# Performance work log

Hardware: AMD Instinct MI355X
Metric: run time of the kernel (lower is better)

Reference implementation:

```python
import jax, jax.numpy as jnp
import numpy as np

B, SM, SI, D, H, FF = 4, 1024, 4096, 256, 8, 1024
EPS = 1e-6

def _ln(x, g, b):
    m = jnp.mean(x, axis=-1, keepdims=True)
    v = jnp.mean(jnp.square(x - m), axis=-1, keepdims=True)
    return (x - m) * jax.lax.rsqrt(v + EPS) * g + b

def setup_inputs() -> dict:
    key = jax.random.key(0)
    ks = jax.random.split(key, 12)
    s = 0.02
    return {
        "state_seq": jax.random.normal(ks[0], (B, SM, D), jnp.float32),
        "input_seq": jax.random.normal(ks[1], (B, SI, D), jnp.float32),
        "Wk": jax.random.normal(ks[2], (D, D), jnp.float32) * s,
        "bk": jnp.zeros((D,), jnp.float32),
        "Wv": jax.random.normal(ks[3], (D, D), jnp.float32) * s,
        "bv": jnp.zeros((D,), jnp.float32),
        "Wq": jax.random.normal(ks[4], (H, D, D), jnp.float32) * s,
        "bq": jnp.zeros((H, D), jnp.float32),
        "Wo": jax.random.normal(ks[5], (H * D, D), jnp.float32) * s,
        "bo": jnp.zeros((D,), jnp.float32),
        "ln1_g": jnp.ones((D,), jnp.float32),
        "ln1_b": jnp.zeros((D,), jnp.float32),
        "W_in": jax.random.normal(ks[6], (D, FF), jnp.float32) * s,
        "b_in": jnp.zeros((FF,), jnp.float32),
        "Wg_nl": jax.random.normal(ks[7], (FF, FF), jnp.float32) * s,
        "bg_nl": jnp.zeros((FF,), jnp.float32),
        "Wg_l": jax.random.normal(ks[8], (FF, FF), jnp.float32) * s,
        "bg_l": jnp.zeros((FF,), jnp.float32),
        "Wg_o": jax.random.normal(ks[9], (FF, D), jnp.float32) * s,
        "bg_o": jnp.zeros((D,), jnp.float32),
        "ln2_g": jnp.ones((D,), jnp.float32),
        "ln2_b": jnp.zeros((D,), jnp.float32),
    }

def reference(state_seq, input_seq, Wk, bk, Wv, bv, Wq, bq, Wo, bo,
              ln1_g, ln1_b, W_in, b_in, Wg_nl, bg_nl, Wg_l, bg_l, Wg_o, bg_o,
              ln2_g, ln2_b):
    # shared key/value projections (multi-query: one K/V, many Q)
    ik = input_seq @ Wk + bk            # [B,SI,D]
    mk = state_seq @ Wk + bk            # [B,SM,D]
    iv = input_seq @ Wv + bv            # [B,SI,D]
    mv = state_seq @ Wv + bv            # [B,SM,D]
    # per-head queries from memory cells, stacked over H
    q = jnp.einsum('bmd,hde->hbme', state_seq, Wq) + bq[:, None, None, :]  # [H,B,SM,D]
    input_score = jnp.einsum('hbme,bse->hbms', q, ik)                      # [H,B,SM,SI]
    self_score = jnp.sum(q * mk[None], axis=-1, keepdims=True)             # [H,B,SM,1]
    score = jnp.concatenate([self_score, input_score], axis=-1)
    score = score / jnp.sqrt(jnp.asarray(D, score.dtype))
    attn = jax.nn.softmax(score, axis=-1)                                  # [H,B,SM,1+SI]
    val = jnp.einsum('hbms,bse->hbme', attn[..., 1:], iv) + attn[..., 0:1] * mv[None]
    concat = jnp.transpose(val, (1, 2, 0, 3)).reshape(val.shape[1], val.shape[2], -1)  # [B,SM,H*D]
    attn_out = concat @ Wo + bo
    x = _ln(attn_out + state_seq, ln1_g, ln1_b)
    h = jax.nn.relu(x @ W_in + b_in)                                       # [B,SM,FF]
    g = jax.nn.relu(h @ Wg_nl + bg_nl) * (h @ Wg_l + bg_l)
    ff = g @ Wg_o + bg_o
    return _ln(ff + x, ln2_g, ln2_b)
```

## Files before the change

kernel.cpp:

```cpp
#include <hip/hip_runtime.h>
#include <hip/hip_bf16.h>

typedef __bf16 bfx8 __attribute__((ext_vector_type(8)));
typedef __bf16 bfx4 __attribute__((ext_vector_type(4)));
typedef float  f32x4 __attribute__((ext_vector_type(4)));
typedef float  f32x16 __attribute__((ext_vector_type(16)));

#define MFMA16(a,b,c) __builtin_amdgcn_mfma_f32_16x16x32_bf16((a),(b),(c),0,0,0)
#define MFMA32(a,b,c) __builtin_amdgcn_mfma_f32_32x32x16_bf16((a),(b),(c),0,0,0)


#define PSCALE 0.09016844f
#define PCLAMP 43.2808512f

__device__ __forceinline__ unsigned cvtpk_bf16(float lo, float hi) {
  unsigned d;
  asm("v_cvt_pk_bf16_f32 %0, %1, %2" : "=v"(d) : "v"(lo), "v"(hi));
  return d;
}

__device__ __forceinline__ bfx8 packswap(const float* p) {
  unsigned a = cvtpk_bf16(p[0], p[1]);
  unsigned b = cvtpk_bf16(p[2], p[3]);
  unsigned c = cvtpk_bf16(p[4], p[5]);
  unsigned d = cvtpk_bf16(p[6], p[7]);
  asm("v_permlane32_swap_b32 %0, %1" : "+v"(a), "+v"(c));
  asm("v_permlane32_swap_b32 %0, %1" : "+v"(b), "+v"(d));
  union { unsigned u[4]; bfx8 v; } uu;
  uu.u[0] = a; uu.u[1] = b; uu.u[2] = c; uu.u[3] = d;
  return uu.v;
}

__device__ __forceinline__ void tile_tr(const float* __restrict__ src, __bf16* __restrict__ dst,
                                        int R, int C, int tile, float (*lt)[65]) {
  int tpr = C >> 6;
  int tr = tile / tpr, tc = tile % tpr;
  int c  = threadIdx.x & 63;
  int r0 = (threadIdx.x >> 6) << 4;
  const float* sp = src + (long)(tr * 64 + r0) * C + tc * 64 + c;
#pragma unroll
  for (int i = 0; i < 16; i++) lt[r0 + i][c] = sp[(long)i * C];
  __syncthreads();
  __bf16* dp = dst + (long)(tc * 64 + r0) * R + tr * 64 + c;
#pragma unroll
  for (int i = 0; i < 16; i++) dp[(long)i * R] = (__bf16)lt[c][r0 + i];
}

__global__ void trans_attn_t(const float* __restrict__ Wk, const float* __restrict__ Wv,
                             const float* __restrict__ Wq, const float* __restrict__ Wo,
                             __bf16* __restrict__ wkvqt, __bf16* __restrict__ wot) {
  __shared__ float lt[64][65];
  int t = blockIdx.x;
  if (t < 16)       tile_tr(Wk, wkvqt, 256, 256, t, lt);
  else if (t < 32)  tile_tr(Wv, wkvqt + 65536, 256, 256, t - 16, lt);
  else if (t < 160) {
    int e = t - 32, m = e >> 4;
    tile_tr(Wq + (long)m * 65536, wkvqt + 131072 + (long)m * 65536, 256, 256, e & 15, lt);
  } else            tile_tr(Wo, wot, 2048, 256, t - 160, lt);
}

__global__ void trans_ffn_t(const float* __restrict__ W_in, const float* __restrict__ Wg_nl,
                            const float* __restrict__ Wg_l, const float* __restrict__ Wg_o,
                            __bf16* __restrict__ dst) {
  __shared__ float lt[64][65];
  int t = blockIdx.x;
  if (t < 64)       tile_tr(W_in, dst, 256, 1024, t, lt);
  else if (t < 320) tile_tr(Wg_nl, dst + 262144, 1024, 1024, t - 64, lt);
  else if (t < 576) tile_tr(Wg_l, dst + 1310720, 1024, 1024, t - 320, lt);
  else              tile_tr(Wg_o, dst + 2359296, 1024, 256, t - 576, lt);
}

__device__ __forceinline__
void gemm_body(const __bf16* __restrict__ Xb, const float* __restrict__ Xf,
               const __bf16* __restrict__ Wt,
               const float* __restrict__ b1, const float* __restrict__ b2,
               const float* __restrict__ b3,
               __bf16* __restrict__ C, __bf16* __restrict__ C2, __bf16* __restrict__ C3,
               float* __restrict__ Cf,
               int M, int N, int Kfull, int kspan, int xmode, int mode, int act,
               int bx, int by, int bz, __bf16* xs, __bf16* wsm) {
  const int tid  = threadIdx.x;
  const int lane = tid & 63;
  const int w    = tid >> 6;
  const int l15  = lane & 15;
  const int quad = lane >> 4;
  const int wm   = (w >> 1) * 64;
  const int wn   = (w & 1) * 64;
  const int m0   = bx * 128;
  const int n0   = by * 128;
  const int k0   = (mode == 7) ? bz * kspan : 0;

  f32x4 acc[4][4];
#pragma unroll
  for (int i = 0; i < 4; i++)
#pragma unroll
    for (int j = 0; j < 4; j++) acc[i][j] = (f32x4){0.f, 0.f, 0.f, 0.f};

  for (int kk = k0; kk < k0 + kspan; kk += 64) {
    __syncthreads();
#pragma unroll
    for (int rep = 0; rep < 4; rep++) {
      int idx = rep * 256 + tid;
      int row = idx >> 3;
      int g   = idx & 7;
      if (xmode == 1) {
        const float* p = Xf + (long)(m0 + row) * Kfull + kk + g * 8;
        f32x4 a0 = *(const f32x4*)p;
        f32x4 a1 = *(const f32x4*)(p + 4);
        bfx8 v;
#pragma unroll
        for (int j = 0; j < 4; j++) { v[j] = (__bf16)a0[j]; v[4 + j] = (__bf16)a1[j]; }
        *(bfx8*)&xs[row * 72 + g * 8] = v;
      } else if (xmode == 2) {
        const __bf16* p = Xb + (long)(m0 + row) * 2048 + kk + g * 8;
        bfx8 a = *(const bfx8*)p;
        bfx8 bb = *(const bfx8*)(p + 1024);
        bfx8 v;
#pragma unroll
        for (int j = 0; j < 8; j++) v[j] = (__bf16)((float)a[j] * (float)bb[j]);
        *(bfx8*)&xs[row * 72 + g * 8] = v;
      } else {
        *(bfx8*)&xs[row * 72 + g * 8] = *(const bfx8*)(Xb + (long)(m0 + row) * Kfull + kk + g * 8);
      }
      *(bfx8*)&wsm[row * 72 + g * 8] = *(const bfx8*)(Wt + (long)(n0 + row) * Kfull + kk + g * 8);
    }
    __syncthreads();
#pragma unroll
    for (int ks = 0; ks < 2; ks++) {
      bfx8 af[4], bf_[4];
#pragma unroll
      for (int i = 0; i < 4; i++) af[i]  = *(const bfx8*)&xs[(wm + 16 * i + l15) * 72 + ks * 32 + quad * 8];
#pragma unroll
      for (int j = 0; j < 4; j++) bf_[j] = *(const bfx8*)&wsm[(wn + 16 * j + l15) * 72 + ks * 32 + quad * 8];
#pragma unroll
      for (int i = 0; i < 4; i++)
#pragma unroll
        for (int j = 0; j < 4; j++) acc[i][j] = MFMA16(af[i], bf_[j], acc[i][j]);
    }
  }

#pragma unroll
  for (int j = 0; j < 4; j++) {
    int n = n0 + wn + 16 * j + l15;
    float bv;
    if (mode == 4)      bv = (n < 256) ? b1[n] : b2[n - 256];
    else if (mode == 5) bv = (n < 256) ? b1[n] : (n < 512) ? b2[n - 256] : b3[n - 512];
    else if (mode == 6) bv = (n < 1024) ? b1[n] : b2[n - 1024];
    else if (mode == 7) bv = (bz == 0) ? b1[n] : 0.f;
    else                bv = b1[n];
#pragma unroll
    for (int i = 0; i < 4; i++) {
#pragma unroll
      for (int r = 0; r < 4; r++) {
        int m = m0 + wm + 16 * i + quad * 4 + r;
        float v = acc[i][j][r] + bv;
        if (mode == 6) { if (n < 1024) v = fmaxf(v, 0.f); }
        else if (act == 1) v = fmaxf(v, 0.f);
        if (mode == 4) {
          if (n < 256) C[(long)m * 256 + n] = (__bf16)v;
          else {
            int bb_ = m >> 12, si = m & 4095;
            C2[((long)(bb_ * 128 + (si >> 5)) * 256 + (n - 256)) * 32 + (si & 31)] = (__bf16)v;
          }
        } else if (mode == 5) {
          if (n < 256)      C[(long)m * 256 + n] = (__bf16)v;
          else if (n < 512) C2[(long)m * 256 + (n - 256)] = (__bf16)v;
          else {
            int nn = n - 512, hhh = nn >> 8, dd = nn & 255;
            C3[(long)hhh * 1048576 + (long)m * 256 + dd] = (__bf16)v;
          }
        } else if (mode == 7) {
          Cf[(long)bz * M * N + (long)m * N + n] = v;
        } else {
          C[(long)m * N + n] = (__bf16)v;
        }
      }
    }
  }
}

__global__ __launch_bounds__(256)
void gemm_bt(const __bf16* Xb, const float* Xf, const __bf16* Wt,
             const float* b1, const float* b2, const float* b3,
             __bf16* C, __bf16* C2, __bf16* C3, float* Cf,
             int M, int N, int Kfull, int kspan, int xmode, int mode, int act) {
  __shared__ __bf16 xs[128 * 72];
  __shared__ __bf16 wsm[128 * 72];
  gemm_body(Xb, Xf, Wt, b1, b2, b3, C, C2, C3, Cf, M, N, Kfull, kspan, xmode, mode, act,
            blockIdx.x, blockIdx.y, blockIdx.z, xs, wsm);
}

__global__ __launch_bounds__(256)
void proj2(const float* input, const float* state, const __bf16* Wkvqt,
           const float* bk, const float* bv, const float* bq,
           __bf16* ik, __bf16* ivT, __bf16* mk, __bf16* mv, __bf16* qbuf) {
  __shared__ __bf16 xs[128 * 72];
  __shared__ __bf16 wsm[128 * 72];
  int bid = blockIdx.x;
  if (bid < 512) {
    gemm_body(nullptr, input, Wkvqt, bk, bv, nullptr, ik, ivT, nullptr, nullptr,
              16384, 512, 256, 256, 1, 4, 0, bid & 127, bid >> 7, 0, xs, wsm);
  } else {
    int b2 = bid - 512;
    gemm_body(nullptr, state, Wkvqt, bk, bv, bq, mk, mv, qbuf, nullptr,
              4096, 2560, 256, 256, 1, 5, 0, b2 & 31, b2 >> 5, 0, xs, wsm);
  }
}

__global__ __launch_bounds__(256)
void attn_kernel_d(const __bf16* __restrict__ qb,
                   const __bf16* __restrict__ ik,
                   const __bf16* __restrict__ ivT,
                   const __bf16* __restrict__ mk,
                   const __bf16* __restrict__ mv,
                   __bf16* __restrict__ concat) {
  __shared__ __bf16 lk[2][32][264];
  __shared__ __bf16 lvt[2][128][40];

  const int tid  = threadIdx.x;
  const int lane = tid & 63;
  const int w    = tid >> 6;
  const int l31  = lane & 31;
  const int h    = lane >> 5;

  const int m0 = blockIdx.x * 128;
  const int b  = blockIdx.y;
  const int hh = blockIdx.z & 7;
  const int dh = blockIdx.z >> 3;
  const int mw = m0 + w * 32;

  const long qbase  = ((long)hh * 4096 + b * 1024 + mw) * 256;
  const long kvbase = (long)b * 4096 * 256;
  const long vtbase = (long)b * 128 * 8192;
  const long mbase  = ((long)b * 1024 + mw) * 256;

  bfx8 qf[16];
  {
    const __bf16* qrow = qb + qbase + (long)l31 * 256 + h * 8;
#pragma unroll
    for (int kt = 0; kt < 16; kt++) qf[kt] = *(const bfx8*)(qrow + kt * 16);
  }

  float ps_l;
  {
    const __bf16* krow = mk + mbase + (long)l31 * 256 + h * 8;
    float s = 0.f;
#pragma unroll
    for (int kt = 0; kt < 16; kt++) {
      bfx8 kv = *(const bfx8*)(krow + kt * 16);
#pragma unroll
      for (int j = 0; j < 8; j++) s += (float)qf[kt][j] * (float)kv[j];
    }
    s += __shfl_xor(s, 32);
    ps_l = __builtin_amdgcn_exp2f(fminf(s * PSCALE, PCLAMP));
  }

  f32x16 oacc[4];
#pragma unroll
  for (int dt = 0; dt < 4; dt++)
#pragma unroll
    for (int i = 0; i < 16; i++) oacc[dt][i] = 0.f;
  float den_l = 0.f;
  bfx8 pf0c, pf1c;

  f32x16 zz;
#pragma unroll
  for (int i = 0; i < 16; i++) zz[i] = 0.f;

  auto sload_k = [&](int c, bfx8* kreg) {
    const long kb = kvbase + (long)c * 8192;
#pragma unroll
    for (int rep = 0; rep < 4; rep++) {
      int idx = rep * 256 + tid;
      kreg[rep] = *(const bfx8*)(ik + kb + (long)(idx >> 5) * 256 + (idx & 31) * 8);
    }
  };
  auto sload_v = [&](int c, bfx8* vreg) {
    const long vb = vtbase + (long)c * 8192 + (long)dh * 4096;
#pragma unroll
    for (int rep = 0; rep < 2; rep++) {
      int idx = rep * 256 + tid;
      vreg[rep] = *(const bfx8*)(ivT + vb + (long)idx * 8);
    }
  };
  auto sstore_k = [&](int slot, const bfx8* kreg) {
#pragma unroll
    for (int rep = 0; rep < 4; rep++) {
      int idx = rep * 256 + tid;
      *(bfx8*)&lk[slot][idx >> 5][(idx & 31) * 8] = kreg[rep];
    }
  };
  auto sstore_v = [&](int slot, const bfx8* vreg) {
#pragma unroll
    for (int rep = 0; rep < 2; rep++) {
      int idx = rep * 256 + tid;
      *(bfx8*)&lvt[slot][idx >> 2][(idx & 3) * 8] = vreg[rep];
    }
  };

  auto chunkMFMA = [&](int vslot, int kslot, bool doS, bool doPV, f32x16* sa) {
#pragma unroll
    for (int t = 0; t < 8; t++) {
      bfx8 vf0, vf1, kf0, kf1;
      if (doPV && t < 4) {
        vf0 = *(const bfx8*)&lvt[vslot][t * 32 + l31][h * 8];
        vf1 = *(const bfx8*)&lvt[vslot][t * 32 + l31][16 + h * 8];
      }
      if (doS) {
        kf0 = *(const bfx8*)&lk[kslot][l31][(2 * t) * 16 + h * 8];
        kf1 = *(const bfx8*)&lk[kslot][l31][(2 * t + 1) * 16 + h * 8];
      }
      if (doPV && t < 4) oacc[t] = MFMA32(pf0c, vf0, oacc[t]);
      if (doS) {
        if (t < 2) sa[2 * t] = MFMA32(kf0, qf[2 * t], zz);
        else       sa[(2 * t) & 3] = MFMA32(kf0, qf[2 * t], sa[(2 * t) & 3]);
      }
      if (doPV && t < 4) oacc[t] = MFMA32(pf1c, vf1, oacc[t]);
      if (doS) {
        if (t < 2) sa[2 * t + 1] = MFMA32(kf1, qf[2 * t + 1], zz);
        else       sa[(2 * t + 1) & 3] = MFMA32(kf1, qf[2 * t + 1], sa[(2 * t + 1) & 3]);
      }
    }
  };

  auto finishP = [&](const f32x16* sa) {
    float p[16];
#pragma unroll
    for (int r = 0; r < 16; r++) {
      float s = (sa[0][r] + sa[1][r]) + (sa[2][r] + sa[3][r]);
      p[r] = __builtin_amdgcn_exp2f(fminf(s * PSCALE, PCLAMP));
      den_l += p[r];
    }
    pf0c = packswap(p);
    pf1c = packswap(p + 8);
  };

  {
    bfx8 kreg[4], vreg[2];
    sload_k(0, kreg);
    sload_v(0, vreg);
    sstore_k(0, kreg);
    sstore_v(0, vreg);
    sload_k(1, kreg);
    sstore_k(1, kreg);
  }
  __syncthreads();

  f32x16 sa[4];
  chunkMFMA(0, 0, true, false, sa);
  finishP(sa);
  __syncthreads();

  for (int i = 0; i < 126; i++) {
    bfx8 kreg[4], vreg[2];
    sload_k(i + 2, kreg);
    sload_v(i + 1, vreg);
    chunkMFMA(i & 1, (i + 1) & 1, true, true, sa);
    sstore_k(i & 1, kreg);
    sstore_v((i + 1) & 1, vreg);
    finishP(sa);
    __syncthreads();
  }
  {
    bfx8 vreg[2];
    sload_v(127, vreg);
    chunkMFMA(0, 1, true, true, sa);
    sstore_v(1, vreg);
    finishP(sa);
    __syncthreads();
  }
  chunkMFMA(1, 0, false, true, sa);

  float tot = den_l + __shfl_xor(den_l, 32) + ps_l;
#pragma unroll
  for (int r = 0; r < 16; r++) {
    int row = (r & 3) + 8 * (r >> 2) + 4 * h;
    float ps   = __shfl(ps_l, row);
    float dinv = 1.f / __shfl(tot, row);
    const __bf16* mvrow = mv + mbase + (long)row * 256 + dh * 128;
    __bf16* crow = concat + ((long)(b * 1024 + mw + row)) * 2048 + hh * 256 + dh * 128;
#pragma unroll
    for (int dt = 0; dt < 4; dt++) {
      int d = dt * 32 + l31;
      crow[d] = (__bf16)((oacc[dt][r] + ps * (float)mvrow[d]) * dinv);
    }
  }
}

__global__ __launch_bounds__(256)
void attn_kernel_f(const __bf16* __restrict__ qb, const __bf16* __restrict__ ik,
                   const __bf16* __restrict__ ivT, const __bf16* __restrict__ mk,
                   const __bf16* __restrict__ mv, __bf16* __restrict__ concat) {
  __shared__ __bf16 lk[2][32][264];
  __shared__ __bf16 lvt[2][256][40];

  const int tid  = threadIdx.x;
  const int lane = tid & 63;
  const int w    = tid >> 6;
  const int l31  = lane & 31;
  const int h    = lane >> 5;

  const int m0 = blockIdx.x * 128;
  const int b  = blockIdx.y;
  const int hh = blockIdx.z;
  const int mw = m0 + w * 32;

  const long qbase  = ((long)hh * 4096 + b * 1024 + mw) * 256;
  const long kvbase = (long)b * 4096 * 256;
  const long vtbase = (long)b * 128 * 8192;
  const long mbase  = ((long)b * 1024 + mw) * 256;

  bfx8 qf[16];
  {
    const __bf16* qrow = qb + qbase + (long)l31 * 256 + h * 8;
#pragma unroll
    for (int kt = 0; kt < 16; kt++) qf[kt] = *(const bfx8*)(qrow + kt * 16);
  }

  float ps_l;
  {
    const __bf16* krow = mk + mbase + (long)l31 * 256 + h * 8;
    float s = 0.f;
#pragma unroll
    for (int kt = 0; kt < 16; kt++) {
      bfx8 kv = *(const bfx8*)(krow + kt * 16);
#pragma unroll
      for (int j = 0; j < 8; j++) s += (float)qf[kt][j] * (float)kv[j];
    }
    s += __shfl_xor(s, 32);
    ps_l = __builtin_amdgcn_exp2f(fminf(s * PSCALE, PCLAMP));
  }

  f32x16 oacc[8];
#pragma unroll
  for (int dt = 0; dt < 8; dt++)
#pragma unroll
    for (int i = 0; i < 16; i++) oacc[dt][i] = 0.f;
  float den_l = 0.f;
  bfx8 pf0c, pf1c;

  f32x16 zz;
#pragma unroll
  for (int i = 0; i < 16; i++) zz[i] = 0.f;

  auto sload_k = [&](int c, bfx8* kreg) {
    const long kb = kvbase + (long)c * 8192;
#pragma unroll
    for (int rep = 0; rep < 4; rep++) {
      int idx = rep * 256 + tid;
      kreg[rep] = *(const bfx8*)(ik + kb + (long)(idx >> 5) * 256 + (idx & 31) * 8);
    }
  };
  auto sload_v = [&](int c, bfx8* vreg) {
    const long vb = vtbase + (long)c * 8192;
#pragma unroll
    for (int rep = 0; rep < 4; rep++) {
      int idx = rep * 256 + tid;
      vreg[rep] = *(const bfx8*)(ivT + vb + (long)idx * 8);
    }
  };
  auto sstore_k = [&](int slot, const bfx8* kreg) {
#pragma unroll
    for (int rep = 0; rep < 4; rep++) {
      int idx = rep * 256 + tid;
      *(bfx8*)&lk[slot][idx >> 5][(idx & 31) * 8] = kreg[rep];
    }
  };
  auto sstore_v = [&](int slot, const bfx8* vreg) {
#pragma unroll
    for (int rep = 0; rep < 4; rep++) {
      int idx = rep * 256 + tid;
      *(bfx8*)&lvt[slot][idx >> 2][(idx & 3) * 8] = vreg[rep];
    }
  };

  auto chunkMFMA = [&](int vslot, int kslot, bool doS, bool doPV, f32x16* sa) {
#pragma unroll
    for (int t = 0; t < 8; t++) {
      bfx8 vf0, vf1, kf0, kf1;
      if (doPV) {
        vf0 = *(const bfx8*)&lvt[vslot][t * 32 + l31][h * 8];
        vf1 = *(const bfx8*)&lvt[vslot][t * 32 + l31][16 + h * 8];
      }
      if (doS) {
        kf0 = *(const bfx8*)&lk[kslot][l31][(2 * t) * 16 + h * 8];
        kf1 = *(const bfx8*)&lk[kslot][l31][(2 * t + 1) * 16 + h * 8];
      }
      if (doPV) oacc[t] = MFMA32(pf0c, vf0, oacc[t]);
      if (doS) {
        if (t < 2) sa[2 * t] = MFMA32(kf0, qf[2 * t], zz);
        else       sa[(2 * t) & 3] = MFMA32(kf0, qf[2 * t], sa[(2 * t) & 3]);
      }
      if (doPV) oacc[t] = MFMA32(pf1c, vf1, oacc[t]);
      if (doS) {
        if (t < 2) sa[2 * t + 1] = MFMA32(kf1, qf[2 * t + 1], zz);
        else       sa[(2 * t + 1) & 3] = MFMA32(kf1, qf[2 * t + 1], sa[(2 * t + 1) & 3]);
      }
    }
  };

  auto finishP = [&](const f32x16* sa) {
    float p[16];
#pragma unroll
    for (int r = 0; r < 16; r++) {
      float s = (sa[0][r] + sa[1][r]) + (sa[2][r] + sa[3][r]);
      p[r] = __builtin_amdgcn_exp2f(fminf(s * PSCALE, PCLAMP));
      den_l += p[r];
    }
    pf0c = packswap(p);
    pf1c = packswap(p + 8);
  };

  {
    bfx8 kreg[4], vreg[4];
    sload_k(0, kreg);
    sload_v(0, vreg);
    sstore_k(0, kreg);
    sstore_v(0, vreg);
    sload_k(1, kreg);
    sstore_k(1, kreg);
  }
  __syncthreads();

  f32x16 sa[4];
  chunkMFMA(0, 0, true, false, sa);
  finishP(sa);
  __syncthreads();

  for (int i = 0; i < 126; i++) {
    bfx8 kreg[4], vreg[4];
    sload_k(i + 2, kreg);
    sload_v(i + 1, vreg);
    chunkMFMA(i & 1, (i + 1) & 1, true, true, sa);
    sstore_k(i & 1, kreg);
    sstore_v((i + 1) & 1, vreg);
    finishP(sa);
    __syncthreads();
  }
  {
    bfx8 vreg[4];
    sload_v(127, vreg);
    chunkMFMA(0, 1, true, true, sa);
    sstore_v(1, vreg);
    finishP(sa);
    __syncthreads();
  }
  chunkMFMA(1, 0, false, true, sa);

  float tot = den_l + __shfl_xor(den_l, 32) + ps_l;
#pragma unroll
  for (int r = 0; r < 16; r++) {
    int row = (r & 3) + 8 * (r >> 2) + 4 * h;
    float ps   = __shfl(ps_l, row);
    float dinv = 1.f / __shfl(tot, row);
    const __bf16* mvrow = mv + mbase + (long)row * 256;
    __bf16* crow = concat + ((long)(b * 1024 + mw + row)) * 2048 + hh * 256;
#pragma unroll
    for (int dt = 0; dt < 8; dt++) {
      int d = dt * 32 + l31;
      crow[d] = (__bf16)((oacc[dt][r] + ps * (float)mvrow[d]) * dinv);
    }
  }
}

__global__ __launch_bounds__(256)
void ln4_kernel(const float* __restrict__ parts, const float* __restrict__ res,
                const float* __restrict__ g, const float* __restrict__ beta,
                __bf16* __restrict__ outb, float* __restrict__ outf) {
  int row  = blockIdx.x * 4 + (threadIdx.x >> 6);
  int lane = threadIdx.x & 63;
  const float* p = parts + (long)row * 256 + lane * 4;
  f32x4 a0 = *(const f32x4*)p;
  f32x4 a1 = *(const f32x4*)(p + 1048576);
  f32x4 a2 = *(const f32x4*)(p + 2097152);
  f32x4 a3 = *(const f32x4*)(p + 3145728);
  f32x4 rv = *(const f32x4*)(res + (long)row * 256 + lane * 4);
  float v[4], s1 = 0.f, s2 = 0.f;
#pragma unroll
  for (int i = 0; i < 4; i++) {
    v[i] = a0[i] + a1[i] + a2[i] + a3[i] + rv[i];
    s1 += v[i];
    s2 += v[i] * v[i];
  }
#pragma unroll
  for (int off = 32; off >= 1; off >>= 1) {
    s1 += __shfl_xor(s1, off);
    s2 += __shfl_xor(s2, off);
  }
  float mean = s1 * (1.f / 256.f);
  float var  = fmaxf(s2 * (1.f / 256.f) - mean * mean, 0.f);
  float rstd = rsqrtf(var + 1e-6f);
#pragma unroll
  for (int i = 0; i < 4; i++) {
    int c = lane * 4 + i;
    float o = (v[i] - mean) * rstd * g[c] + beta[c];
    if (outb) outb[(long)row * 256 + c] = (__bf16)o;
    if (outf) outf[(long)row * 256 + c] = o;
  }
}

extern "C" void kernel_launch(void* const* d_in, const int* in_sizes, int n_in,
                              void* d_out, int out_size, void* d_ws, size_t ws_size,
                              hipStream_t stream) {
  const float* state  = (const float*)d_in[0];
  const float* input  = (const float*)d_in[1];
  const float* Wk     = (const float*)d_in[2];
  const float* bk     = (const float*)d_in[3];
  const float* Wv     = (const float*)d_in[4];
  const float* bv     = (const float*)d_in[5];
  const float* Wq     = (const float*)d_in[6];
  const float* bq     = (const float*)d_in[7];
  const float* Wo     = (const float*)d_in[8];
  const float* bo     = (const float*)d_in[9];
  const float* ln1g   = (const float*)d_in[10];
  const float* ln1b   = (const float*)d_in[11];
  const float* W_in   = (const float*)d_in[12];
  const float* b_in   = (const float*)d_in[13];
  const float* Wg_nl  = (const float*)d_in[14];
  const float* bg_nl  = (const float*)d_in[15];
  const float* Wg_l   = (const float*)d_in[16];
  const float* bg_l   = (const float*)d_in[17];
  const float* Wg_o   = (const float*)d_in[18];
  const float* bg_o   = (const float*)d_in[19];
  const float* ln2g   = (const float*)d_in[20];
  const float* ln2b   = (const float*)d_in[21];
  float* out = (float*)d_out;

  const size_t needed_elems = 28442624;
  if (ws_size < needed_elems * sizeof(__bf16)) return;

  __bf16* ws = (__bf16*)d_ws;
  size_t off = 0;
  auto alloc = [&](size_t n) { __bf16* p = ws + off; off += n; return p; };
  __bf16* Wkvqt  = alloc(655360);
  __bf16* Wot    = alloc(524288);
  __bf16* ik     = alloc(4194304);
  __bf16* ivT    = alloc(4194304);
  __bf16* mk     = alloc(1048576);
  __bf16* mv     = alloc(1048576);
  __bf16* qbuf   = alloc(8388608);
  __bf16* concat = alloc(8388608);
  float*  wo_parts = (float*)qbuf;
  __bf16* x      = mv;
  __bf16* hbuf   = ik;
  __bf16* t12    = qbuf;
  float*  ff_parts = (float*)ik;
  __bf16* Wffn   = concat;
  float*  xf     = (float*)(concat + 3670016);

  static int useD = -1;
  if (useD < 0) {
    hipFuncAttributes fa{};
    hipError_t e = hipFuncGetAttributes(&fa, (const void*)attn_kernel_d);
    useD = (e == hipSuccess && fa.localSizeBytes <= 16) ? 1 : 0;
  }

  dim3 blk(256);

  trans_attn_t<<<dim3(288), blk, 0, stream>>>(Wk, Wv, Wq, Wo, Wkvqt, Wot);

  proj2<<<dim3(1152), blk, 0, stream>>>(input, state, Wkvqt, bk, bv, bq,
                                        ik, ivT, mk, mv, qbuf);

  if (useD)
    attn_kernel_d<<<dim3(8, 4, 16), blk, 0, stream>>>(qbuf, ik, ivT, mk, mv, concat);
  else
    attn_kernel_f<<<dim3(8, 4, 8), blk, 0, stream>>>(qbuf, ik, ivT, mk, mv, concat);

  gemm_bt<<<dim3(32, 2, 4), blk, 0, stream>>>(concat, nullptr, Wot, bo, nullptr, nullptr,
                                              nullptr, nullptr, nullptr, wo_parts,
                                              4096, 256, 2048, 512, 0, 7, 0);
  ln4_kernel<<<dim3(1024), blk, 0, stream>>>(wo_parts, state, ln1g, ln1b, x, xf);

  trans_ffn_t<<<dim3(640), blk, 0, stream>>>(W_in, Wg_nl, Wg_l, Wg_o, Wffn);

  gemm_bt<<<dim3(32, 8), blk, 0, stream>>>(x, nullptr, Wffn, b_in, nullptr, nullptr,
                                           hbuf, nullptr, nullptr, nullptr,
                                           4096, 1024, 256, 256, 0, 0, 1);
  gemm_bt<<<dim3(32, 16), blk, 0, stream>>>(hbuf, nullptr, Wffn + 262144, bg_nl, bg_l, nullptr,
                                            t12, nullptr, nullptr, nullptr,
                                            4096, 2048, 1024, 1024, 0, 6, 0);
  gemm_bt<<<dim3(32, 2, 4), blk, 0, stream>>>(t12, nullptr, Wffn + 2359296, bg_o, nullptr, nullptr,
                                              nullptr, nullptr, nullptr, ff_parts,
                                              4096, 256, 1024, 256, 2, 7, 0);
  ln4_kernel<<<dim3(1024), blk, 0, stream>>>(ff_parts, xf, ln2g, ln2b, nullptr, out);
}
```

Measured before the change: 547.0 us.

## Specialize attention warps into score and PV roles communicating P via LDS

Replaces the attention kernel, where every wave computed both QK scores and PV products for a half of the head dim, with a warp-specialized variant. Two waves compute scores and softmax numerators and write bf16 P tiles to shared memory, while two other waves consume them to accumulate the full 256-wide output. The aim is to overlap the exp/softmax work with MFMA on the PV side, avoid recomputing scores for each head-dim half, and use waves_per_eu hints to raise register budget. The cost is extra LDS traffic, an added barrier per chunk, and halved rows per block.

```diff
diff --git a/kernel.cpp b/kernel.cpp
--- a/kernel.cpp
+++ b/kernel.cpp
@@ -207,66 +207,35 @@
   }
 }
 
-__global__ __launch_bounds__(256)
-void attn_kernel_d(const __bf16* __restrict__ qb,
+__global__ __attribute__((amdgpu_flat_work_group_size(256, 256)))
+__attribute__((amdgpu_waves_per_eu(2, 2)))
+void attn_kernel_s(const __bf16* __restrict__ qb,
                    const __bf16* __restrict__ ik,
                    const __bf16* __restrict__ ivT,
                    const __bf16* __restrict__ mk,
                    const __bf16* __restrict__ mv,
                    __bf16* __restrict__ concat) {
   __shared__ __bf16 lk[2][32][264];
-  __shared__ __bf16 lvt[2][128][40];
+  __shared__ __bf16 lvt[2][256][40];
+  __shared__ __bf16 pl[2][64][16];
 
   const int tid  = threadIdx.x;
   const int lane = tid & 63;
   const int w    = tid >> 6;
+  const int role = w >> 1;
+  const int grp  = w & 1;
   const int l31  = lane & 31;
   const int h    = lane >> 5;
 
-  const int m0 = blockIdx.x * 128;
+  const int m0 = blockIdx.x * 64;
   const int b  = blockIdx.y;
-  const int hh = blockIdx.z & 7;
-  const int dh = blockIdx.z >> 3;
-  const int mw = m0 + w * 32;
-
-  const long qbase  = ((long)hh * 4096 + b * 1024 + mw) * 256;
+  const int hh = blockIdx.z;
+  const int mw = m0 + grp * 32;
+
   const long kvbase = (long)b * 4096 * 256;
   const long vtbase = (long)b * 128 * 8192;
   const long mbase  = ((long)b * 1024 + mw) * 256;
 
-  bfx8 qf[16];
-  {
-    const __bf16* qrow = qb + qbase + (long)l31 * 256 + h * 8;
-#pragma unroll
-    for (int kt = 0; kt < 16; kt++) qf[kt] = *(const bfx8*)(qrow + kt * 16);
-  }
-
-  float ps_l;
-  {
-    const __bf16* krow = mk + mbase + (long)l31 * 256 + h * 8;
-    float s = 0.f;
-#pragma unroll
-    for (int kt = 0; kt < 16; kt++) {
-      bfx8 kv = *(const bfx8*)(krow + kt * 16);
-#pragma unroll
-      for (int j = 0; j < 8; j++) s += (float)qf[kt][j] * (float)kv[j];
-    }
-    s += __shfl_xor(s, 32);
-    ps_l = __builtin_amdgcn_exp2f(fminf(s * PSCALE, PCLAMP));
-  }
-
-  f32x16 oacc[4];
-#pragma unroll
-  for (int dt = 0; dt < 4; dt++)
-#pragma unroll
-    for (int i = 0; i < 16; i++) oacc[dt][i] = 0.f;
-  float den_l = 0.f;
-  bfx8 pf0c, pf1c;
-
-  f32x16 zz;
-#pragma unroll
-  for (int i = 0; i < 16; i++) zz[i] = 0.f;
-
   auto sload_k = [&](int c, bfx8* kreg) {
     const long kb = kvbase + (long)c * 8192;
 #pragma unroll
@@ -276,9 +245,9 @@
     }
   };
   auto sload_v = [&](int c, bfx8* vreg) {
-    const long vb = vtbase + (long)c * 8192 + (long)dh * 4096;
-#pragma unroll
-    for (int rep = 0; rep < 2; rep++) {
+    const long vb = vtbase + (long)c * 8192;
+#pragma unroll
+    for (int rep = 0; rep < 4; rep++) {
       int idx = rep * 256 + tid;
       vreg[rep] = *(const bfx8*)(ivT + vb + (long)idx * 8);
     }
@@ -292,97 +261,180 @@
   };
   auto sstore_v = [&](int slot, const bfx8* vreg) {
 #pragma unroll
-    for (int rep = 0; rep < 2; rep++) {
+    for (int rep = 0; rep < 4; rep++) {
       int idx = rep * 256 + tid;
       *(bfx8*)&lvt[slot][idx >> 2][(idx & 3) * 8] = vreg[rep];
     }
   };
 
-  auto chunkMFMA = [&](int vslot, int kslot, bool doS, bool doPV, f32x16* sa) {
-#pragma unroll
-    for (int t = 0; t < 8; t++) {
-      bfx8 vf0, vf1, kf0, kf1;
-      if (doPV && t < 4) {
-        vf0 = *(const bfx8*)&lvt[vslot][t * 32 + l31][h * 8];
-        vf1 = *(const bfx8*)&lvt[vslot][t * 32 + l31][16 + h * 8];
-      }
-      if (doS) {
-        kf0 = *(const bfx8*)&lk[kslot][l31][(2 * t) * 16 + h * 8];
-        kf1 = *(const bfx8*)&lk[kslot][l31][(2 * t + 1) * 16 + h * 8];
-      }
-      if (doPV && t < 4) oacc[t] = MFMA32(pf0c, vf0, oacc[t]);
-      if (doS) {
-        if (t < 2) sa[2 * t] = MFMA32(kf0, qf[2 * t], zz);
-        else       sa[(2 * t) & 3] = MFMA32(kf0, qf[2 * t], sa[(2 * t) & 3]);
-      }
-      if (doPV && t < 4) oacc[t] = MFMA32(pf1c, vf1, oacc[t]);
-      if (doS) {
-        if (t < 2) sa[2 * t + 1] = MFMA32(kf1, qf[2 * t + 1], zz);
-        else       sa[(2 * t + 1) & 3] = MFMA32(kf1, qf[2 * t + 1], sa[(2 * t + 1) & 3]);
-      }
-    }
-  };
-
-  auto finishP = [&](const f32x16* sa) {
-    float p[16];
+  float* ex = (float*)&pl[0][0][0];
+
+  if (role == 0) {
+    bfx8 qf[16];
+    {
+      const long qbase = ((long)hh * 4096 + b * 1024 + mw) * 256;
+      const __bf16* qrow = qb + qbase + (long)l31 * 256 + h * 8;
+#pragma unroll
+      for (int kt = 0; kt < 16; kt++) qf[kt] = *(const bfx8*)(qrow + kt * 16);
+    }
+    float ps_l;
+    {
+      const __bf16* krow = mk + mbase + (long)l31 * 256 + h * 8;
+      float s = 0.f;
+#pragma unroll
+      for (int kt = 0; kt < 16; kt++) {
+        bfx8 kv = *(const bfx8*)(krow + kt * 16);
+#pragma unroll
+        for (int j = 0; j < 8; j++) s += (float)qf[kt][j] * (float)kv[j];
+      }
+      s += __shfl_xor(s, 32);
+      ps_l = __builtin_amdgcn_exp2f(fminf(s * PSCALE, PCLAMP));
+    }
+
+    f32x16 zz;
+#pragma unroll
+    for (int i = 0; i < 16; i++) zz[i] = 0.f;
+    f32x16 sa[4];
+    float den_l = 0.f;
+
+    auto chunkS = [&](int kslot) {
+#pragma unroll
+      for (int t = 0; t < 8; t++) {
+        bfx8 kf0 = *(const bfx8*)&lk[kslot][l31][(2 * t) * 16 + h * 8];
+        bfx8 kf1 = *(const bfx8*)&lk[kslot][l31][(2 * t + 1) * 16 + h * 8];
+        if (t < 2) {
+          sa[2 * t]     = MFMA32(kf0, qf[2 * t], zz);
+          sa[2 * t + 1] = MFMA32(kf1, qf[2 * t + 1], zz);
+        } else {
+          sa[(2 * t) & 3]     = MFMA32(kf0, qf[2 * t], sa[(2 * t) & 3]);
+          sa[(2 * t + 1) & 3] = MFMA32(kf1, qf[2 * t + 1], sa[(2 * t + 1) & 3]);
+        }
+      }
+    };
+    auto finishP = [&]() {
+      float p[16];
+#pragma unroll
+      for (int r = 0; r < 16; r++) {
+        float s = (sa[0][r] + sa[1][r]) + (sa[2][r] + sa[3][r]);
+        p[r] = __builtin_amdgcn_exp2f(fminf(s * PSCALE, PCLAMP));
+        den_l += p[r];
+      }
+      bfx8 pf0 = packswap(p);
+      bfx8 pf1 = packswap(p + 8);
+      *(bfx8*)&pl[grp][lane][0] = pf0;
+      *(bfx8*)&pl[grp][lane][8] = pf1;
+    };
+
+    {
+      bfx8 kreg[4], vreg[4];
+      sload_k(0, kreg);
+      sload_v(0, vreg);
+      sstore_k(0, kreg);
+      sstore_v(0, vreg);
+      sload_k(1, kreg);
+      sstore_k(1, kreg);
+    }
+    __syncthreads();
+    chunkS(0);
+    finishP();
+    __syncthreads();
+
+    for (int i = 0; i < 126; i++) {
+      bfx8 kreg[4], vreg[4];
+      sload_k(i + 2, kreg);
+      sload_v(i + 1, vreg);
+      __syncthreads();
+      chunkS((i + 1) & 1);
+      sstore_k(i & 1, kreg);
+      sstore_v((i + 1) & 1, vreg);
+      finishP();
+      __syncthreads();
+    }
+    {
+      bfx8 vreg[4];
+      sload_v(127, vreg);
+      __syncthreads();
+      chunkS(1);
+      sstore_v(1, vreg);
+      finishP();
+      __syncthreads();
+    }
+    __syncthreads();
+    float den_row = den_l + __shfl_xor(den_l, 32);
+    ex[grp * 32 + l31]      = den_row + ps_l;
+    ex[64 + grp * 32 + l31] = ps_l;
+    __syncthreads();
+  } else {
+    f32x16 oacc[8];
+#pragma unroll
+    for (int dt = 0; dt < 8; dt++)
+#pragma unroll
+      for (int i = 0; i < 16; i++) oacc[dt][i] = 0.f;
+    bfx8 pf0c, pf1c;
+
+    auto pfload = [&]() {
+      pf0c = *(const bfx8*)&pl[grp][lane][0];
+      pf1c = *(const bfx8*)&pl[grp][lane][8];
+    };
+    auto chunkPV = [&](int vslot) {
+#pragma unroll
+      for (int t = 0; t < 8; t++) {
+        bfx8 vf0 = *(const bfx8*)&lvt[vslot][t * 32 + l31][h * 8];
+        bfx8 vf1 = *(const bfx8*)&lvt[vslot][t * 32 + l31][16 + h * 8];
+        oacc[t] = MFMA32(pf0c, vf0, oacc[t]);
+        oacc[t] = MFMA32(pf1c, vf1, oacc[t]);
+      }
+    };
+
+    {
+      bfx8 kreg[4], vreg[4];
+      sload_k(0, kreg);
+      sload_v(0, vreg);
+      sstore_k(0, kreg);
+      sstore_v(0, vreg);
+      sload_k(1, kreg);
+      sstore_k(1, kreg);
+    }
+    __syncthreads();
+    __syncthreads();
+
+    for (int i = 0; i < 126; i++) {
+      bfx8 kreg[4], vreg[4];
+      sload_k(i + 2, kreg);
+      sload_v(i + 1, vreg);
+      pfload();
+      __syncthreads();
+      chunkPV(i & 1);
+      sstore_k(i & 1, kreg);
+      sstore_v((i + 1) & 1, vreg);
+      __syncthreads();
+    }
+    {
+      bfx8 vreg[4];
+      sload_v(127, vreg);
+      pfload();
+      __syncthreads();
+      chunkPV(0);
+      sstore_v(1, vreg);
+      __syncthreads();
+    }
+    pfload();
+    __syncthreads();
+    chunkPV(1);
+    __syncthreads();
+
 #pragma unroll
     for (int r = 0; r < 16; r++) {
-      float s = (sa[0][r] + sa[1][r]) + (sa[2][r] + sa[3][r]);
-      p[r] = __builtin_amdgcn_exp2f(fminf(s * PSCALE, PCLAMP));
-      den_l += p[r];
-    }
-    pf0c = packswap(p);
-    pf1c = packswap(p + 8);
-  };
-
-  {
-    bfx8 kreg[4], vreg[2];
-    sload_k(0, kreg);
-    sload_v(0, vreg);
-    sstore_k(0, kreg);
-    sstore_v(0, vreg);
-    sload_k(1, kreg);
-    sstore_k(1, kreg);
-  }
-  __syncthreads();
-
-  f32x16 sa[4];
-  chunkMFMA(0, 0, true, false, sa);
-  finishP(sa);
-  __syncthreads();
-
-  for (int i = 0; i < 126; i++) {
-    bfx8 kreg[4], vreg[2];
-    sload_k(i + 2, kreg);
-    sload_v(i + 1, vreg);
-    chunkMFMA(i & 1, (i + 1) & 1, true, true, sa);
-    sstore_k(i & 1, kreg);
-    sstore_v((i + 1) & 1, vreg);
-    finishP(sa);
-    __syncthreads();
-  }
-  {
-    bfx8 vreg[2];
-    sload_v(127, vreg);
-    chunkMFMA(0, 1, true, true, sa);
-    sstore_v(1, vreg);
-    finishP(sa);
-    __syncthreads();
-  }
-  chunkMFMA(1, 0, false, true, sa);
-
-  float tot = den_l + __shfl_xor(den_l, 32) + ps_l;
-#pragma unroll
-  for (int r = 0; r < 16; r++) {
-    int row = (r & 3) + 8 * (r >> 2) + 4 * h;
-    float ps   = __shfl(ps_l, row);
-    float dinv = 1.f / __shfl(tot, row);
-    const __bf16* mvrow = mv + mbase + (long)row * 256 + dh * 128;
-    __bf16* crow = concat + ((long)(b * 1024 + mw + row)) * 2048 + hh * 256 + dh * 128;
-#pragma unroll
-    for (int dt = 0; dt < 4; dt++) {
-      int d = dt * 32 + l31;
-      crow[d] = (__bf16)((oacc[dt][r] + ps * (float)mvrow[d]) * dinv);
+      int row = (r & 3) + 8 * (r >> 2) + 4 * h;
+      float dinv = 1.f / ex[grp * 32 + row];
+      float ps   = ex[64 + grp * 32 + row];
+      const __bf16* mvrow = mv + mbase + (long)row * 256;
+      __bf16* crow = concat + ((long)(b * 1024 + mw + row)) * 2048 + hh * 256;
+#pragma unroll
+      for (int dt = 0; dt < 8; dt++) {
+        int d = dt * 32 + l31;
+        crow[d] = (__bf16)((oacc[dt][r] + ps * (float)mvrow[d]) * dinv);
+      }
     }
   }
 }
@@ -648,11 +700,11 @@
   __bf16* Wffn   = concat;
   float*  xf     = (float*)(concat + 3670016);
 
-  static int useD = -1;
-  if (useD < 0) {
+  static int useS = -1;
+  if (useS < 0) {
     hipFuncAttributes fa{};
-    hipError_t e = hipFuncGetAttributes(&fa, (const void*)attn_kernel_d);
-    useD = (e == hipSuccess && fa.localSizeBytes <= 16) ? 1 : 0;
+    hipError_t e = hipFuncGetAttributes(&fa, (const void*)attn_kernel_s);
+    useS = (e == hipSuccess && fa.localSizeBytes <= 16) ? 1 : 0;
   }
 
   dim3 blk(256);
@@ -662,8 +714,8 @@
   proj2<<<dim3(1152), blk, 0, stream>>>(input, state, Wkvqt, bk, bv, bq,
                                         ik, ivT, mk, mv, qbuf);
 
-  if (useD)
-    attn_kernel_d<<<dim3(8, 4, 16), blk, 0, stream>>>(qbuf, ik, ivT, mk, mv, concat);
+  if (useS)
+    attn_kernel_s<<<dim3(16, 4, 8), blk, 0, stream>>>(qbuf, ik, ivT, mk, mv, concat);
   else
     attn_kernel_f<<<dim3(8, 4, 8), blk, 0, stream>>>(qbuf, ik, ivT, mk, mv, concat);
 
```

Result: faster. 489.9 us (-10.4%).
